# Kernel optimization log

Measured on AMD Instinct MI355X. Metric: run time of the kernel, lower is better.

## Reference

```python
import jax, jax.numpy as jnp
import numpy as np

B, L, D, E, K = 8, 384, 1024, 4, 2
H = 4 * D  # expert MLP hidden


def setup_inputs() -> dict:
    key = jax.random.key(0)
    ks = jax.random.split(key, 10)
    def w(k, shape, fan_in):
        return jax.random.normal(k, shape, jnp.float32) / np.sqrt(fan_in).astype(np.float32)
    return {
        "context_c": jax.random.normal(ks[0], (B, L, D), jnp.float32),
        "time_cond": jax.random.normal(ks[1], (B, D), jnp.float32),
        "gate_W": w(ks[2], (E, 3 * D), 3 * D),
        "gate_b": jnp.zeros((E,), jnp.float32),
        "tmod_W": w(ks[3], (2 * E, D), D),
        "tmod_b": jnp.zeros((2 * E,), jnp.float32),
        "eW1": w(ks[4], (E, D, H), D),
        "eb1": jnp.zeros((E, H), jnp.float32),
        "eW2": w(ks[5], (E, H, D), H),
        "eb2": jnp.zeros((E, D), jnp.float32),
        "sW1": w(ks[6], (D, H), D),
        "sb1": jnp.zeros((H,), jnp.float32),
        "sW2": w(ks[7], (H, D), H),
        "sb2": jnp.zeros((D,), jnp.float32),
    }


def reference(context_c, time_cond, gate_W, gate_b, tmod_W, tmod_b,
              eW1, eb1, eW2, eb2, sW1, sb1, sW2, sb2):
    Lh = Lw = L // 3
    Lp = L - Lh - Lw
    head = context_c[:, :Lh]            # (B, Lh, D)
    wrist = context_c[:, Lh:Lh + Lw]    # (B, Lw, D)
    prop = context_c[:, Lh + Lw:]       # (B, Lp, D)

    # per-sample modality-combo aggregates for the gate
    full_agg = context_c.mean(axis=1)
    hp_agg = (head.sum(axis=1) + prop.sum(axis=1)) / (Lh + Lp)
    wp_agg = (wrist.sum(axis=1) + prop.sum(axis=1)) / (Lw + Lp)
    gate_in = jnp.concatenate([full_agg, hp_agg, wp_agg], axis=-1)  # (B, 3D)

    logits = gate_in @ gate_W.T + gate_b                            # (B, E)
    mod = jax.nn.silu(time_cond) @ tmod_W.T + tmod_b                # (B, 2E)
    scale, shift = mod[:, :E], mod[:, E:]
    logits = logits * (1.0 + scale) + shift

    scores = jax.nn.softmax(logits, axis=-1)
    tw, ti = jax.lax.top_k(scores, K)                               # (B, K)
    tw = tw / (tw.sum(axis=-1, keepdims=True) + 1e-8)
    # per-sample combined weight for each expert: (B, E)
    w_be = (jax.nn.one_hot(ti, E, dtype=tw.dtype) * tw[..., None]).sum(axis=1)

    # modality mask per expert (E, L): expert 1 skips wrist, expert 2 skips head
    mask_np = np.ones((E, L), np.float32)
    mask_np[1, Lh:Lh + Lw] = 0.0
    mask_np[2, :Lh] = 0.0
    mask = jnp.asarray(mask_np)

    # run all experts on all tokens (token-wise MLP), combine with per-sample
    # routing weights and per-expert modality masks — identical math to the
    # original per-sample sliced dispatch.
    h = jax.nn.gelu(jnp.einsum('bld,edh->belh', context_c, eW1)
                    + eb1[None, :, None, :], approximate=True)      # (B,E,L,H)
    y = jnp.einsum('belh,ehd->beld', h, eW2) + eb2[None, :, None, :]
    out = jnp.einsum('be,el,beld->bld', w_be, mask, y)

    # shared expert (always-on)
    shared = jax.nn.gelu(context_c @ sW1 + sb1, approximate=True) @ sW2 + sb2
    return out + shared
```

## Files before the change

### kernel.cpp

```cpp
#include <hip/hip_runtime.h>
#include <cstdint>
#include <cstddef>


#define DEV __device__ __forceinline__

typedef __attribute__((ext_vector_type(8))) __bf16 bf16x8;
typedef __attribute__((ext_vector_type(4))) __bf16 bf16x4;
typedef __attribute__((ext_vector_type(4))) float f32x4;

static constexpr int Bb = 8, Ll = 384, Dd = 1024, Ee = 4, Hh = 4096;

DEV void load_lds16(const void* g, void* l) {
  __builtin_amdgcn_global_load_lds(
      (const __attribute__((address_space(1))) void*)g,
      (__attribute__((address_space(3))) void*)l, 16, 0, 0);
}

DEV float gelu_tanh(float x) {
  float u = 0.7978845608028654f * (x + 0.044715f * x * x * x);
  float t = 1.0f - 2.0f / (1.0f + __expf(2.0f * u));
  return 0.5f * x * (1.0f + t);
}

DEV float wave_red(float v) {
#pragma unroll
  for (int o = 32; o > 0; o >>= 1) v += __shfl_down(v, o, 64);
  return v;
}


__global__ void cvt_x_kernel(const float* __restrict__ src, __bf16* __restrict__ dst, int n4) {
  int i = blockIdx.x * blockDim.x + threadIdx.x;
  if (i >= n4) return;
  float4 v = ((const float4*)src)[i];
  bf16x4 o;
  o.x = (__bf16)v.x; o.y = (__bf16)v.y; o.z = (__bf16)v.z; o.w = (__bf16)v.w;
  ((bf16x4*)dst)[i] = o;
}

__global__ void transpose_cvt_kernel(const float* __restrict__ src, __bf16* __restrict__ dst,
                                     int nr, int nc) {
  __shared__ float t[32][33];
  size_t base = (size_t)blockIdx.z * nr * nc;
  src += base; dst += base;
  int x = threadIdx.x & 31, y = threadIdx.x >> 5;
  int c0 = blockIdx.x * 32, r0 = blockIdx.y * 32;
#pragma unroll
  for (int r = 0; r < 4; ++r) {
    int rr = y + r * 8;
    t[rr][x] = src[(size_t)(r0 + rr) * nc + c0 + x];
  }
  __syncthreads();
#pragma unroll
  for (int r = 0; r < 4; ++r) {
    int rr = y + r * 8;
    dst[(size_t)(c0 + rr) * nr + r0 + x] = (__bf16)t[x][rr];
  }
}


__global__ void agg_kernel(const float* __restrict__ ctx, float* __restrict__ part) {
  int c = blockIdx.x, b = blockIdx.y, t = threadIdx.x;
  int d0 = t * 4;
  float4 sum = {0.f, 0.f, 0.f, 0.f};
  const float* p = ctx + ((size_t)(b * Ll + c * 64)) * Dd + d0;
  for (int l = 0; l < 64; ++l) {
    float4 v = *(const float4*)(p + (size_t)l * Dd);
    sum.x += v.x; sum.y += v.y; sum.z += v.z; sum.w += v.w;
  }
  *(float4*)(part + ((size_t)(b * 6 + c)) * Dd + d0) = sum;
}

__global__ void gate_kernel(const float* __restrict__ part, const float* __restrict__ tc,
                            const float* __restrict__ gW, const float* __restrict__ gb,
                            const float* __restrict__ tW, const float* __restrict__ tb,
                            int* __restrict__ slotE, float* __restrict__ slotW) {
  __shared__ float gi[3 * Dd];
  __shared__ float st[Dd];
  __shared__ float red[12];
  int b = blockIdx.x, t = threadIdx.x;
  const float* pb = part + (size_t)b * 6 * Dd;
#pragma unroll
  for (int k = 0; k < 4; ++k) {
    int d = t * 4 + k;
    float p0 = pb[d], p1 = pb[Dd + d], p2 = pb[2 * Dd + d];
    float p3 = pb[3 * Dd + d], p4 = pb[4 * Dd + d], p5 = pb[5 * Dd + d];
    gi[d]          = (p0 + p1 + p2 + p3 + p4 + p5) * (1.0f / 384.0f);
    gi[Dd + d]     = (p0 + p1 + p4 + p5) * (1.0f / 256.0f);
    gi[2 * Dd + d] = (p2 + p3 + p4 + p5) * (1.0f / 256.0f);
    float tv = tc[b * Dd + d];
    st[d] = tv / (1.0f + __expf(-tv));
  }
  __syncthreads();
  int wid = t >> 6, lane = t & 63;
  float aL = 0.f;
  for (int i = lane; i < 3 * Dd; i += 64) aL += gi[i] * gW[wid * 3 * Dd + i];
  aL = wave_red(aL);
  float aA = 0.f, aB = 0.f;
  for (int i = lane; i < Dd; i += 64) {
    float s = st[i];
    aA += s * tW[wid * Dd + i];
    aB += s * tW[(wid + 4) * Dd + i];
  }
  aA = wave_red(aA); aB = wave_red(aB);
  if (lane == 0) { red[wid] = aL; red[4 + wid] = aA; red[8 + wid] = aB; }
  __syncthreads();
  if (t == 0) {
    float lg[4];
#pragma unroll
    for (int e = 0; e < 4; ++e) {
      float logit = red[e] + gb[e];
      float scale = red[4 + e] + tb[e];
      float shift = red[8 + e] + tb[4 + e];
      lg[e] = logit * (1.0f + scale) + shift;
    }
    float m = fmaxf(fmaxf(lg[0], lg[1]), fmaxf(lg[2], lg[3]));
    float p[4], sum = 0.f;
#pragma unroll
    for (int e = 0; e < 4; ++e) { p[e] = __expf(lg[e] - m); sum += p[e]; }
#pragma unroll
    for (int e = 0; e < 4; ++e) p[e] /= sum;
    int i0 = 0;
    for (int e = 1; e < 4; ++e) if (p[e] > p[i0]) i0 = e;
    int i1 = -1;
    for (int e = 0; e < 4; ++e) if (e != i0 && (i1 < 0 || p[e] > p[i1])) i1 = e;
    float sw = p[i0] + p[i1] + 1e-8f;
    slotE[b * 4 + 0] = i0; slotE[b * 4 + 1] = i1;
    slotW[b * 4 + 0] = p[i0] / sw; slotW[b * 4 + 1] = p[i1] / sw;
  }
}


__global__ __launch_bounds__(256) void gemm1_kernel(
    const __bf16* __restrict__ Xbf, const __bf16* __restrict__ W1T,
    const __bf16* __restrict__ S1T, const float* __restrict__ eb1,
    const float* __restrict__ sb1, const int* __restrict__ slotE,
    const float* __restrict__ slotW, __bf16* __restrict__ Hbuf, int bbase) {
  constexpr int K = Dd;
  int nt = blockIdx.x, mt = blockIdx.y, z = blockIdx.z;
  int bl = z / 3, s = z - bl * 3;
  int b = bbase + bl;
  int e = (s == 2) ? Ee : slotE[b * 4 + s];
  if ((e == 1 && mt == 1) || (e == 2 && mt == 0)) return;
  float wgt = (s == 2) ? 1.0f : slotW[b * 4 + s];

  const __bf16* Ab = Xbf + ((size_t)(b * Ll + mt * 128)) * K;
  const __bf16* Bbp = (e < Ee ? W1T + (size_t)e * Hh * K : S1T) + (size_t)(nt * 128) * K;
  const float* b1p = (e < Ee ? eb1 + e * Hh : sb1);

  __shared__ __align__(16) char smem[34816];

  int tid = threadIdx.x, wid = tid >> 6, lane = tid & 63;
  int q = lane >> 4, l16 = lane & 15;
  int wm = wid >> 1, wn = wid & 1;

  const __bf16* gp[8];
  uint32_t lo[8];
#pragma unroll
  for (int u = 0; u < 8; ++u) {
    int c = wid * 8 + u;
    int isB = c >> 4;
    int blk = (c & 15) >> 1;
    int ks = c & 1;
    const __bf16* base = isB ? Bbp : Ab;
    gp[u] = base + (size_t)(blk * 16 + l16) * K + ks * 32 + q * 8;
    lo[u] = (uint32_t)(isB * 16384 + (blk * 2 + ks) * 1024);
  }

  f32x4 acc[4][4];
  f32x4 zero = {0.f, 0.f, 0.f, 0.f};
#pragma unroll
  for (int i = 0; i < 4; ++i)
#pragma unroll
    for (int j = 0; j < 4; ++j) acc[i][j] = zero;

  for (int kt = 0; kt < K / 64; ++kt) {
    __syncthreads();
#pragma unroll
    for (int u = 0; u < 8; ++u) load_lds16(gp[u], smem + lo[u]);
    __syncthreads();
#pragma unroll
    for (int ks = 0; ks < 2; ++ks) {
      bf16x8 a[4], bb[4];
#pragma unroll
      for (int i = 0; i < 4; ++i)
        a[i] = *(const bf16x8*)(smem + (((wm * 4 + i) * 2 + ks) * 64 + lane) * 16);
#pragma unroll
      for (int j = 0; j < 4; ++j)
        bb[j] = *(const bf16x8*)(smem + 16384 + (((wn * 4 + j) * 2 + ks) * 64 + lane) * 16);
#pragma unroll
      for (int i = 0; i < 4; ++i)
#pragma unroll
        for (int j = 0; j < 4; ++j)
          acc[i][j] = __builtin_amdgcn_mfma_f32_16x16x32_bf16(a[i], bb[j], acc[i][j], 0, 0, 0);
    }
#pragma unroll
    for (int u = 0; u < 8; ++u) gp[u] += 64;
  }

  float bias[4];
#pragma unroll
  for (int j = 0; j < 4; ++j) bias[j] = b1p[nt * 128 + wn * 64 + j * 16 + l16];

  __syncthreads();
  __bf16* tile = (__bf16*)smem;
#pragma unroll
  for (int i = 0; i < 4; ++i)
#pragma unroll
    for (int j = 0; j < 4; ++j)
#pragma unroll
      for (int r = 0; r < 4; ++r) {
        float x = acc[i][j][r] + bias[j];
        int row = wm * 64 + i * 16 + q * 4 + r;
        int col = wn * 64 + j * 16 + l16;
        tile[row * 136 + col] = (__bf16)(wgt * gelu_tanh(x));
      }
  __syncthreads();
  __bf16* Hrow = Hbuf + ((size_t)(bl * 3 + s) * Ll + mt * 128) * Hh + nt * 128;
#pragma unroll
  for (int t2 = 0; t2 < 8; ++t2) {
    int gidx = t2 * 256 + tid;
    int row = gidx >> 4, cg = gidx & 15;
    bf16x8 v = *(const bf16x8*)(tile + row * 136 + cg * 8);
    *(bf16x8*)(Hrow + (size_t)row * Hh + cg * 8) = v;
  }
}


__global__ __launch_bounds__(256) void gemm2_kernel(
    const __bf16* __restrict__ Hbuf, const __bf16* __restrict__ W2T,
    const __bf16* __restrict__ S2T, const float* __restrict__ eb2,
    const float* __restrict__ sb2, const int* __restrict__ slotE,
    const float* __restrict__ slotW, float* __restrict__ out,
    __bf16* __restrict__ pbuf, int bbase, int bc) {
  constexpr int K = Hh;
  constexpr int KC = 1024;
  int nt = blockIdx.x, mt = blockIdx.y, z = blockIdx.z;
  int kc = z & 3, bl = z >> 2;
  int b = bbase + bl;

  __shared__ __align__(16) char smem[34816];

  int tid = threadIdx.x, wid = tid >> 6, lane = tid & 63;
  int q = lane >> 4, l16 = lane & 15;
  int wm = wid >> 1, wn = wid & 1;

  f32x4 acc[4][4];
  f32x4 zero = {0.f, 0.f, 0.f, 0.f};
#pragma unroll
  for (int i = 0; i < 4; ++i)
#pragma unroll
    for (int j = 0; j < 4; ++j) acc[i][j] = zero;
  float biasacc[4] = {0.f, 0.f, 0.f, 0.f};

  for (int s = 0; s < 3; ++s) {
    int e = (s == 2) ? Ee : slotE[b * 4 + s];
    if ((e == 1 && mt == 1) || (e == 2 && mt == 0)) continue;
    float wgt = (s == 2) ? 1.0f : slotW[b * 4 + s];

    const __bf16* Ab = Hbuf + ((size_t)(bl * 3 + s) * Ll + mt * 128) * K + (size_t)kc * KC;
    const __bf16* Bbp = (e < Ee ? W2T + (size_t)e * Dd * K : S2T) + (size_t)(nt * 128) * K + (size_t)kc * KC;

    const __bf16* gp[8];
    uint32_t lo[8];
#pragma unroll
    for (int u = 0; u < 8; ++u) {
      int c = wid * 8 + u;
      int isB = c >> 4;
      int blk = (c & 15) >> 1;
      int ks = c & 1;
      const __bf16* base = isB ? Bbp : Ab;
      gp[u] = base + (size_t)(blk * 16 + l16) * K + ks * 32 + q * 8;
      lo[u] = (uint32_t)(isB * 16384 + (blk * 2 + ks) * 1024);
    }

    for (int kt = 0; kt < KC / 64; ++kt) {
      __syncthreads();
#pragma unroll
      for (int u = 0; u < 8; ++u) load_lds16(gp[u], smem + lo[u]);
      __syncthreads();
#pragma unroll
      for (int ks = 0; ks < 2; ++ks) {
        bf16x8 a[4], bb[4];
#pragma unroll
        for (int i = 0; i < 4; ++i)
          a[i] = *(const bf16x8*)(smem + (((wm * 4 + i) * 2 + ks) * 64 + lane) * 16);
#pragma unroll
        for (int j = 0; j < 4; ++j)
          bb[j] = *(const bf16x8*)(smem + 16384 + (((wn * 4 + j) * 2 + ks) * 64 + lane) * 16);
#pragma unroll
        for (int i = 0; i < 4; ++i)
#pragma unroll
          for (int j = 0; j < 4; ++j)
            acc[i][j] = __builtin_amdgcn_mfma_f32_16x16x32_bf16(a[i], bb[j], acc[i][j], 0, 0, 0);
      }
#pragma unroll
      for (int u = 0; u < 8; ++u) gp[u] += 64;
    }

    if (kc == 0) {
      const float* b2p = (e < Ee ? eb2 + e * Dd : sb2);
#pragma unroll
      for (int j = 0; j < 4; ++j)
        biasacc[j] += wgt * b2p[nt * 128 + wn * 64 + j * 16 + l16];
    }
  }

  if (pbuf) {
    __syncthreads();
    __bf16* tile = (__bf16*)smem;
#pragma unroll
    for (int i = 0; i < 4; ++i)
#pragma unroll
      for (int j = 0; j < 4; ++j)
#pragma unroll
        for (int r = 0; r < 4; ++r) {
          int row = wm * 64 + i * 16 + q * 4 + r;
          int col = wn * 64 + j * 16 + l16;
          tile[row * 136 + col] = (__bf16)(acc[i][j][r] + biasacc[j]);
        }
    __syncthreads();
    __bf16* Prow = pbuf + (((size_t)(kc * bc + bl) * Ll + mt * 128)) * Dd + nt * 128;
#pragma unroll
    for (int t2 = 0; t2 < 8; ++t2) {
      int gidx = t2 * 256 + tid;
      int row = gidx >> 4, cg = gidx & 15;
      bf16x8 v = *(const bf16x8*)(tile + row * 136 + cg * 8);
      *(bf16x8*)(Prow + (size_t)row * Dd + cg * 8) = v;
    }
  } else {
    float* orow = out + ((size_t)(b * Ll + mt * 128)) * Dd + nt * 128;
#pragma unroll
    for (int i = 0; i < 4; ++i)
#pragma unroll
      for (int j = 0; j < 4; ++j)
#pragma unroll
        for (int r = 0; r < 4; ++r) {
          int row = wm * 64 + i * 16 + q * 4 + r;
          int col = wn * 64 + j * 16 + l16;
          atomicAdd(orow + (size_t)row * Dd + col, acc[i][j][r] + biasacc[j]);
        }
  }
}

__global__ void reduce4_kernel(const __bf16* __restrict__ pbuf, float* __restrict__ out,
                               int n8, size_t stride) {
  int i = blockIdx.x * blockDim.x + threadIdx.x;
  if (i >= n8) return;
  size_t base = (size_t)i * 8;
  float sum[8];
#pragma unroll
  for (int k = 0; k < 8; ++k) sum[k] = 0.f;
#pragma unroll
  for (int kc = 0; kc < 4; ++kc) {
    bf16x8 v = *(const bf16x8*)(pbuf + kc * stride + base);
#pragma unroll
    for (int k = 0; k < 8; ++k) sum[k] += (float)v[k];
  }
  float4 o0 = {sum[0], sum[1], sum[2], sum[3]};
  float4 o1 = {sum[4], sum[5], sum[6], sum[7]};
  *(float4*)(out + base) = o0;
  *(float4*)(out + base + 4) = o1;
}


extern "C" void kernel_launch(void* const* d_in, const int* in_sizes, int n_in,
                              void* d_out, int out_size, void* d_ws, size_t ws_size,
                              hipStream_t stream) {
  (void)in_sizes; (void)n_in;
  const float* ctx = (const float*)d_in[0];
  const float* tc  = (const float*)d_in[1];
  const float* gW  = (const float*)d_in[2];
  const float* gb  = (const float*)d_in[3];
  const float* tW  = (const float*)d_in[4];
  const float* tb  = (const float*)d_in[5];
  const float* eW1 = (const float*)d_in[6];
  const float* eb1 = (const float*)d_in[7];
  const float* eW2 = (const float*)d_in[8];
  const float* eb2 = (const float*)d_in[9];
  const float* sW1 = (const float*)d_in[10];
  const float* sb1 = (const float*)d_in[11];
  const float* sW2 = (const float*)d_in[12];
  const float* sb2 = (const float*)d_in[13];
  float* out = (float*)d_out;

  char* ws = (char*)d_ws;
  size_t off = 0;
  auto alloc = [&](size_t sz) { size_t o = off; off += (sz + 255) & ~(size_t)255; return o; };
  size_t oW1T = alloc((size_t)Ee * Hh * Dd * 2);
  size_t oW2T = alloc((size_t)Ee * Dd * Hh * 2);
  size_t oS1T = alloc((size_t)Hh * Dd * 2);
  size_t oS2T = alloc((size_t)Dd * Hh * 2);
  size_t oX   = alloc((size_t)Bb * Ll * Dd * 2);
  size_t oP   = alloc((size_t)Bb * 6 * Dd * 4);
  size_t oSE  = alloc(Bb * 4 * sizeof(int));
  size_t oSW  = alloc(Bb * 4 * sizeof(float));
  size_t fixed = off;

  auto hbufB = [&](int bc) { return (size_t)bc * 3 * Ll * Hh * 2; };
  auto pbufB = [&](int bc) { return (size_t)4 * bc * Ll * Dd * 2; };
  int bc = 1; bool use_pbuf = false;
  if (fixed + hbufB(8) + pbufB(8) + 512 <= ws_size)      { bc = 8; use_pbuf = true; }
  else if (fixed + hbufB(4) + pbufB(4) + 512 <= ws_size) { bc = 4; use_pbuf = true; }
  else if (fixed + hbufB(4) + 512 <= ws_size)            { bc = 4; use_pbuf = false; }
  else if (fixed + hbufB(2) + 512 <= ws_size)            { bc = 2; use_pbuf = false; }
  else                                                   { bc = 1; use_pbuf = false; }
  int nchunk = Bb / bc;
  size_t oH = alloc(hbufB(bc));
  size_t oPB = use_pbuf ? alloc(pbufB(bc)) : 0;

  __bf16* W1T = (__bf16*)(ws + oW1T);
  __bf16* W2T = (__bf16*)(ws + oW2T);
  __bf16* S1T = (__bf16*)(ws + oS1T);
  __bf16* S2T = (__bf16*)(ws + oS2T);
  __bf16* Xbf = (__bf16*)(ws + oX);
  float*  part = (float*)(ws + oP);
  int*    slotE = (int*)(ws + oSE);
  float*  slotW = (float*)(ws + oSW);
  __bf16* Hbuf = (__bf16*)(ws + oH);
  __bf16* Pbuf = use_pbuf ? (__bf16*)(ws + oPB) : nullptr;

  hipMemsetAsync(d_out, 0, (size_t)out_size * sizeof(float), stream);

  cvt_x_kernel<<<(Bb * Ll * Dd / 4 + 255) / 256, 256, 0, stream>>>(ctx, Xbf, Bb * Ll * Dd / 4);
  transpose_cvt_kernel<<<dim3(Hh / 32, Dd / 32, Ee), 256, 0, stream>>>(eW1, W1T, Dd, Hh);
  transpose_cvt_kernel<<<dim3(Dd / 32, Hh / 32, Ee), 256, 0, stream>>>(eW2, W2T, Hh, Dd);
  transpose_cvt_kernel<<<dim3(Hh / 32, Dd / 32, 1), 256, 0, stream>>>(sW1, S1T, Dd, Hh);
  transpose_cvt_kernel<<<dim3(Dd / 32, Hh / 32, 1), 256, 0, stream>>>(sW2, S2T, Hh, Dd);
  agg_kernel<<<dim3(6, Bb), 256, 0, stream>>>(ctx, part);
  gate_kernel<<<Bb, 256, 0, stream>>>(part, tc, gW, gb, tW, tb, slotE, slotW);

  for (int c = 0; c < nchunk; ++c) {
    gemm1_kernel<<<dim3(Hh / 128, 3, bc * 3), 256, 0, stream>>>(
        Xbf, W1T, S1T, eb1, sb1, slotE, slotW, Hbuf, c * bc);
    gemm2_kernel<<<dim3(Dd / 128, 3, bc * 4), 256, 0, stream>>>(
        Hbuf, W2T, S2T, eb2, sb2, slotE, slotW, out, Pbuf, c * bc, bc);
    if (use_pbuf) {
      int n8 = bc * Ll * Dd / 8;
      reduce4_kernel<<<(n8 + 255) / 256, 256, 0, stream>>>(
          Pbuf, out + (size_t)c * bc * Ll * Dd, n8, (size_t)bc * Ll * Dd);
    }
  }
}
```

Baseline: 604.6 us.

## Double-buffer LDS in both GEMMs and balance gemm2 split-K across active slots

Both GEMM kernels now use a 64KB double-buffered LDS so the next K-tile's global-to-LDS loads are issued before the current tile's MFMAs, with one barrier per iteration instead of two. gemm2 flattens all active slots' K ranges into one tile sequence and splits it evenly across the four kc blocks, so skipped slots no longer leave blocks idle. The output memset is skipped when the partial-buffer reduction path writes the output. The larger LDS footprint cuts the number of resident blocks per CU, and the single barrier depends on the async LDS loads completing in time.

```diff
diff --git a/kernel.cpp b/kernel.cpp
--- a/kernel.cpp
+++ b/kernel.cpp
@@ -149,7 +149,7 @@
   const __bf16* Bbp = (e < Ee ? W1T + (size_t)e * Hh * K : S1T) + (size_t)(nt * 128) * K;
   const float* b1p = (e < Ee ? eb1 + e * Hh : sb1);
 
-  __shared__ __align__(16) char smem[34816];
+  __shared__ __align__(16) char smem[65536];
 
   int tid = threadIdx.x, wid = tid >> 6, lane = tid & 63;
   int q = lane >> 4, l16 = lane & 15;
@@ -175,28 +175,36 @@
 #pragma unroll
     for (int j = 0; j < 4; ++j) acc[i][j] = zero;
 
-  for (int kt = 0; kt < K / 64; ++kt) {
+#pragma unroll
+  for (int u = 0; u < 8; ++u) load_lds16(gp[u], smem + lo[u]);
+
+  constexpr int NK = K / 64;
+  for (int kt = 0; kt < NK; ++kt) {
+    int ph = kt & 1;
     __syncthreads();
-#pragma unroll
-    for (int u = 0; u < 8; ++u) load_lds16(gp[u], smem + lo[u]);
-    __syncthreads();
+    if (kt + 1 < NK) {
+#pragma unroll
+      for (int u = 0; u < 8; ++u) {
+        gp[u] += 64;
+        load_lds16(gp[u], smem + lo[u] + (ph ^ 1) * 32768);
+      }
+    }
+    const char* sm = (const char*)smem + ph * 32768;
 #pragma unroll
     for (int ks = 0; ks < 2; ++ks) {
       bf16x8 a[4], bb[4];
 #pragma unroll
       for (int i = 0; i < 4; ++i)
-        a[i] = *(const bf16x8*)(smem + (((wm * 4 + i) * 2 + ks) * 64 + lane) * 16);
+        a[i] = *(const bf16x8*)(sm + (((wm * 4 + i) * 2 + ks) * 64 + lane) * 16);
 #pragma unroll
       for (int j = 0; j < 4; ++j)
-        bb[j] = *(const bf16x8*)(smem + 16384 + (((wn * 4 + j) * 2 + ks) * 64 + lane) * 16);
+        bb[j] = *(const bf16x8*)(sm + 16384 + (((wn * 4 + j) * 2 + ks) * 64 + lane) * 16);
 #pragma unroll
       for (int i = 0; i < 4; ++i)
 #pragma unroll
         for (int j = 0; j < 4; ++j)
           acc[i][j] = __builtin_amdgcn_mfma_f32_16x16x32_bf16(a[i], bb[j], acc[i][j], 0, 0, 0);
     }
-#pragma unroll
-    for (int u = 0; u < 8; ++u) gp[u] += 64;
   }
 
   float bias[4];
@@ -235,75 +243,109 @@
     const float* __restrict__ slotW, float* __restrict__ out,
     __bf16* __restrict__ pbuf, int bbase, int bc) {
   constexpr int K = Hh;
-  constexpr int KC = 1024;
   int nt = blockIdx.x, mt = blockIdx.y, z = blockIdx.z;
   int kc = z & 3, bl = z >> 2;
   int b = bbase + bl;
 
-  __shared__ __align__(16) char smem[34816];
+  __shared__ __align__(16) char smem[65536];
 
   int tid = threadIdx.x, wid = tid >> 6, lane = tid & 63;
   int q = lane >> 4, l16 = lane & 15;
   int wm = wid >> 1, wn = wid & 1;
 
-  f32x4 acc[4][4];
-  f32x4 zero = {0.f, 0.f, 0.f, 0.f};
-#pragma unroll
-  for (int i = 0; i < 4; ++i)
-#pragma unroll
-    for (int j = 0; j < 4; ++j) acc[i][j] = zero;
+  const __bf16 *A0 = nullptr, *A1 = nullptr, *A2 = nullptr;
+  const __bf16 *B0 = nullptr, *B1 = nullptr, *B2 = nullptr;
   float biasacc[4] = {0.f, 0.f, 0.f, 0.f};
-
+  int nact = 0;
+#pragma unroll
   for (int s = 0; s < 3; ++s) {
     int e = (s == 2) ? Ee : slotE[b * 4 + s];
-    if ((e == 1 && mt == 1) || (e == 2 && mt == 0)) continue;
-    float wgt = (s == 2) ? 1.0f : slotW[b * 4 + s];
-
-    const __bf16* Ab = Hbuf + ((size_t)(bl * 3 + s) * Ll + mt * 128) * K + (size_t)kc * KC;
-    const __bf16* Bbp = (e < Ee ? W2T + (size_t)e * Dd * K : S2T) + (size_t)(nt * 128) * K + (size_t)kc * KC;
-
-    const __bf16* gp[8];
-    uint32_t lo[8];
+    bool skip = (e == 1 && mt == 1) || (e == 2 && mt == 0);
+    if (!skip) {
+      const __bf16* Ap = Hbuf + ((size_t)(bl * 3 + s) * Ll + mt * 128) * K;
+      const __bf16* Bp = (e < Ee ? W2T + (size_t)e * Dd * K : S2T) + (size_t)(nt * 128) * K;
+      if (nact == 0)      { A0 = Ap; B0 = Bp; }
+      else if (nact == 1) { A1 = Ap; B1 = Bp; }
+      else                { A2 = Ap; B2 = Bp; }
+      if (kc == 0) {
+        float wgt = (s == 2) ? 1.0f : slotW[b * 4 + s];
+        const float* b2p = (e < Ee ? eb2 + e * Dd : sb2);
+#pragma unroll
+        for (int j = 0; j < 4; ++j)
+          biasacc[j] += wgt * b2p[nt * 128 + wn * 64 + j * 16 + l16];
+      }
+      ++nact;
+    }
+  }
+
+  int quarter = (nact * 64) >> 2;
+  int f0 = kc * quarter, f1 = f0 + quarter;
+
+  uint32_t lo[8];
+#pragma unroll
+  for (int u = 0; u < 8; ++u) {
+    int c = wid * 8 + u;
+    int isB = c >> 4;
+    int blk = (c & 15) >> 1;
+    int ks = c & 1;
+    lo[u] = (uint32_t)(isB * 16384 + (blk * 2 + ks) * 1024);
+  }
+
+  const __bf16* gp[8];
+  auto setupPtrs = [&](int ft) {
+    int sl = ft >> 6, kt = ft & 63;
+    const __bf16* Ap = (sl == 0) ? A0 : ((sl == 1) ? A1 : A2);
+    const __bf16* Bp = (sl == 0) ? B0 : ((sl == 1) ? B1 : B2);
 #pragma unroll
     for (int u = 0; u < 8; ++u) {
       int c = wid * 8 + u;
       int isB = c >> 4;
       int blk = (c & 15) >> 1;
       int ks = c & 1;
-      const __bf16* base = isB ? Bbp : Ab;
-      gp[u] = base + (size_t)(blk * 16 + l16) * K + ks * 32 + q * 8;
-      lo[u] = (uint32_t)(isB * 16384 + (blk * 2 + ks) * 1024);
-    }
-
-    for (int kt = 0; kt < KC / 64; ++kt) {
-      __syncthreads();
-#pragma unroll
-      for (int u = 0; u < 8; ++u) load_lds16(gp[u], smem + lo[u]);
-      __syncthreads();
-#pragma unroll
-      for (int ks = 0; ks < 2; ++ks) {
-        bf16x8 a[4], bb[4];
-#pragma unroll
-        for (int i = 0; i < 4; ++i)
-          a[i] = *(const bf16x8*)(smem + (((wm * 4 + i) * 2 + ks) * 64 + lane) * 16);
+      const __bf16* base = isB ? Bp : Ap;
+      gp[u] = base + (size_t)(blk * 16 + l16) * K + ks * 32 + q * 8 + (size_t)kt * 64;
+    }
+  };
+
+  f32x4 acc[4][4];
+  f32x4 zero = {0.f, 0.f, 0.f, 0.f};
+#pragma unroll
+  for (int i = 0; i < 4; ++i)
+#pragma unroll
+    for (int j = 0; j < 4; ++j) acc[i][j] = zero;
+
+  setupPtrs(f0);
+#pragma unroll
+  for (int u = 0; u < 8; ++u) load_lds16(gp[u], smem + lo[u]);
+
+  for (int ft = f0; ft < f1; ++ft) {
+    int ph = (ft - f0) & 1;
+    __syncthreads();
+    if (ft + 1 < f1) {
+      if (((ft + 1) & 63) == 0) {
+        setupPtrs(ft + 1);
+      } else {
+#pragma unroll
+        for (int u = 0; u < 8; ++u) gp[u] += 64;
+      }
+#pragma unroll
+      for (int u = 0; u < 8; ++u) load_lds16(gp[u], smem + lo[u] + (ph ^ 1) * 32768);
+    }
+    const char* sm = (const char*)smem + ph * 32768;
+#pragma unroll
+    for (int ks = 0; ks < 2; ++ks) {
+      bf16x8 a[4], bb[4];
+#pragma unroll
+      for (int i = 0; i < 4; ++i)
+        a[i] = *(const bf16x8*)(sm + (((wm * 4 + i) * 2 + ks) * 64 + lane) * 16);
+#pragma unroll
+      for (int j = 0; j < 4; ++j)
+        bb[j] = *(const bf16x8*)(sm + 16384 + (((wn * 4 + j) * 2 + ks) * 64 + lane) * 16);
+#pragma unroll
+      for (int i = 0; i < 4; ++i)
 #pragma unroll
         for (int j = 0; j < 4; ++j)
-          bb[j] = *(const bf16x8*)(smem + 16384 + (((wn * 4 + j) * 2 + ks) * 64 + lane) * 16);
-#pragma unroll
-        for (int i = 0; i < 4; ++i)
-#pragma unroll
-          for (int j = 0; j < 4; ++j)
-            acc[i][j] = __builtin_amdgcn_mfma_f32_16x16x32_bf16(a[i], bb[j], acc[i][j], 0, 0, 0);
-      }
-#pragma unroll
-      for (int u = 0; u < 8; ++u) gp[u] += 64;
-    }
-
-    if (kc == 0) {
-      const float* b2p = (e < Ee ? eb2 + e * Dd : sb2);
-#pragma unroll
-      for (int j = 0; j < 4; ++j)
-        biasacc[j] += wgt * b2p[nt * 128 + wn * 64 + j * 16 + l16];
+          acc[i][j] = __builtin_amdgcn_mfma_f32_16x16x32_bf16(a[i], bb[j], acc[i][j], 0, 0, 0);
     }
   }
 
@@ -421,7 +463,8 @@
   __bf16* Hbuf = (__bf16*)(ws + oH);
   __bf16* Pbuf = use_pbuf ? (__bf16*)(ws + oPB) : nullptr;
 
-  hipMemsetAsync(d_out, 0, (size_t)out_size * sizeof(float), stream);
+  if (!use_pbuf)
+    hipMemsetAsync(d_out, 0, (size_t)out_size * sizeof(float), stream);
 
   cvt_x_kernel<<<(Bb * Ll * Dd / 4 + 255) / 256, 256, 0, stream>>>(ctx, Xbf, Bb * Ll * Dd / 4);
   transpose_cvt_kernel<<<dim3(Hh / 32, Dd / 32, Ee), 256, 0, stream>>>(eW1, W1T, Dd, Hh);
```

Result: slower. 783.4 us (+29.6%).

## Double-buffer LDS tiles in both expert GEMMs and skip redundant output memset

Applied to the files above, without the earlier changes.

Both GEMM kernels now prefetch the next K-tile into a second LDS buffer with async global-to-LDS loads while MFMAs run on the current buffer. This removes one barrier per K step and overlaps global load latency with compute. The cost is that LDS per block grows from about 34 KB to 64 KB, which lowers how many blocks fit on a CU. The output memset is also skipped when the partial-buffer reduction path writes the output fully.

```diff
diff --git a/kernel.cpp b/kernel.cpp
--- a/kernel.cpp
+++ b/kernel.cpp
@@ -149,7 +149,7 @@
   const __bf16* Bbp = (e < Ee ? W1T + (size_t)e * Hh * K : S1T) + (size_t)(nt * 128) * K;
   const float* b1p = (e < Ee ? eb1 + e * Hh : sb1);
 
-  __shared__ __align__(16) char smem[34816];
+  __shared__ __align__(16) char smem[65536];
 
   int tid = threadIdx.x, wid = tid >> 6, lane = tid & 63;
   int q = lane >> 4, l16 = lane & 15;
@@ -175,28 +175,36 @@
 #pragma unroll
     for (int j = 0; j < 4; ++j) acc[i][j] = zero;
 
-  for (int kt = 0; kt < K / 64; ++kt) {
+#pragma unroll
+  for (int u = 0; u < 8; ++u) load_lds16(gp[u], smem + lo[u]);
+
+  constexpr int NK = K / 64;
+  for (int kt = 0; kt < NK; ++kt) {
+    int ph = kt & 1;
     __syncthreads();
-#pragma unroll
-    for (int u = 0; u < 8; ++u) load_lds16(gp[u], smem + lo[u]);
-    __syncthreads();
+    if (kt + 1 < NK) {
+#pragma unroll
+      for (int u = 0; u < 8; ++u) {
+        gp[u] += 64;
+        load_lds16(gp[u], smem + lo[u] + (ph ^ 1) * 32768);
+      }
+    }
+    const char* sm = (const char*)smem + ph * 32768;
 #pragma unroll
     for (int ks = 0; ks < 2; ++ks) {
       bf16x8 a[4], bb[4];
 #pragma unroll
       for (int i = 0; i < 4; ++i)
-        a[i] = *(const bf16x8*)(smem + (((wm * 4 + i) * 2 + ks) * 64 + lane) * 16);
+        a[i] = *(const bf16x8*)(sm + (((wm * 4 + i) * 2 + ks) * 64 + lane) * 16);
 #pragma unroll
       for (int j = 0; j < 4; ++j)
-        bb[j] = *(const bf16x8*)(smem + 16384 + (((wn * 4 + j) * 2 + ks) * 64 + lane) * 16);
+        bb[j] = *(const bf16x8*)(sm + 16384 + (((wn * 4 + j) * 2 + ks) * 64 + lane) * 16);
 #pragma unroll
       for (int i = 0; i < 4; ++i)
 #pragma unroll
         for (int j = 0; j < 4; ++j)
           acc[i][j] = __builtin_amdgcn_mfma_f32_16x16x32_bf16(a[i], bb[j], acc[i][j], 0, 0, 0);
     }
-#pragma unroll
-    for (int u = 0; u < 8; ++u) gp[u] += 64;
   }
 
   float bias[4];
@@ -240,7 +248,7 @@
   int kc = z & 3, bl = z >> 2;
   int b = bbase + bl;
 
-  __shared__ __align__(16) char smem[34816];
+  __shared__ __align__(16) char smem[65536];
 
   int tid = threadIdx.x, wid = tid >> 6, lane = tid & 63;
   int q = lane >> 4, l16 = lane & 15;
@@ -275,28 +283,36 @@
       lo[u] = (uint32_t)(isB * 16384 + (blk * 2 + ks) * 1024);
     }
 
-    for (int kt = 0; kt < KC / 64; ++kt) {
+#pragma unroll
+    for (int u = 0; u < 8; ++u) load_lds16(gp[u], smem + lo[u]);
+
+    constexpr int NK = KC / 64;
+    for (int kt = 0; kt < NK; ++kt) {
+      int ph = kt & 1;
       __syncthreads();
-#pragma unroll
-      for (int u = 0; u < 8; ++u) load_lds16(gp[u], smem + lo[u]);
-      __syncthreads();
+      if (kt + 1 < NK) {
+#pragma unroll
+        for (int u = 0; u < 8; ++u) {
+          gp[u] += 64;
+          load_lds16(gp[u], smem + lo[u] + (ph ^ 1) * 32768);
+        }
+      }
+      const char* sm = (const char*)smem + ph * 32768;
 #pragma unroll
       for (int ks = 0; ks < 2; ++ks) {
         bf16x8 a[4], bb[4];
 #pragma unroll
         for (int i = 0; i < 4; ++i)
-          a[i] = *(const bf16x8*)(smem + (((wm * 4 + i) * 2 + ks) * 64 + lane) * 16);
+          a[i] = *(const bf16x8*)(sm + (((wm * 4 + i) * 2 + ks) * 64 + lane) * 16);
 #pragma unroll
         for (int j = 0; j < 4; ++j)
-          bb[j] = *(const bf16x8*)(smem + 16384 + (((wn * 4 + j) * 2 + ks) * 64 + lane) * 16);
+          bb[j] = *(const bf16x8*)(sm + 16384 + (((wn * 4 + j) * 2 + ks) * 64 + lane) * 16);
 #pragma unroll
         for (int i = 0; i < 4; ++i)
 #pragma unroll
           for (int j = 0; j < 4; ++j)
             acc[i][j] = __builtin_amdgcn_mfma_f32_16x16x32_bf16(a[i], bb[j], acc[i][j], 0, 0, 0);
       }
-#pragma unroll
-      for (int u = 0; u < 8; ++u) gp[u] += 64;
     }
 
     if (kc == 0) {
@@ -421,7 +437,8 @@
   __bf16* Hbuf = (__bf16*)(ws + oH);
   __bf16* Pbuf = use_pbuf ? (__bf16*)(ws + oPB) : nullptr;
 
-  hipMemsetAsync(d_out, 0, (size_t)out_size * sizeof(float), stream);
+  if (!use_pbuf)
+    hipMemsetAsync(d_out, 0, (size_t)out_size * sizeof(float), stream);
 
   cvt_x_kernel<<<(Bb * Ll * Dd / 4 + 255) / 256, 256, 0, stream>>>(ctx, Xbf, Bb * Ll * Dd / 4);
   transpose_cvt_kernel<<<dim3(Hh / 32, Dd / 32, Ee), 256, 0, stream>>>(eW1, W1T, Dd, Hh);
```

New measurement: 581.3 us. -3.9%, faster.
